# Kernel tuning notes

Hardware: AMD Instinct MI355X
Metric: run time of the kernel (lower is better)

Reference implementation:

```python
import jax, jax.numpy as jnp
import numpy as np

B, C, N, M, K = 8, 64, 8192, 2048, 16
FPS_RATIO, TAU = 0.7, 0.2


def setup_inputs() -> dict:
    key = jax.random.key(0)
    k1, k2 = jax.random.split(key)
    x = jax.random.normal(k1, (B, C, N), dtype=jnp.float32)
    pos = jax.random.normal(k2, (B, 3, N), dtype=jnp.float32)
    return {"x": x, "pos": pos, "m": M}


def _fps(pts, key, fps_m):
    # pts: [N, 3] -> farthest point sampling indices [fps_m]
    n = pts.shape[0]
    start = jax.random.randint(key, (), 0, n)
    d0 = jnp.full((n,), 1e10, dtype=jnp.float32)

    def step(carry, _):
        dist, last = carry
        d = jnp.sum((pts - pts[last]) ** 2, axis=1)  # [N]
        dist = jnp.minimum(dist, d)
        far = jnp.argmax(dist)
        return (dist, far), far

    (_, _), cents = jax.lax.scan(step, (d0, start), None, length=fps_m - 1)
    return jnp.concatenate([start[None], cents])


def _hybrid_idx(pos, m, fps_ratio, key):
    # pos: [B, 3, N] -> idx [B, m]  (FPS for fps_m points, random for the rest)
    b, _, n = pos.shape
    fps_m = max(1, int(m * fps_ratio))
    rand_m = m - fps_m
    pts = jnp.transpose(pos, (0, 2, 1))  # [B, N, 3]
    keys = jax.random.split(key, b)
    cents = jax.vmap(lambda p, k: _fps(p, k, fps_m))(pts, keys)  # [B, fps_m]
    if rand_m > 0:
        rkeys = jax.random.split(jax.random.fold_in(key, 1), b)
        rand = jax.vmap(lambda k: jax.random.permutation(k, n)[:rand_m])(rkeys)
        idx = jnp.concatenate([cents, rand], axis=1)
    else:
        idx = cents
    return idx[:, :m]


def _gather_neighbor(feat, idx):
    # feat: [B, C, N], idx: [B, m, k] -> [B, C, m, k]
    return jax.vmap(lambda f, i: f[:, i])(feat, idx)


def reference(x, pos, m):
    b = x.shape[0]
    idx = _hybrid_idx(pos, m, FPS_RATIO, jax.random.key(42))  # [B, m]
    pos_sub = jax.vmap(lambda p, i: p[:, i])(pos, idx)  # [B, 3, m]

    # KNN via squared distances (same ordering as euclidean cdist), no grad path
    ps = jax.lax.stop_gradient(jnp.transpose(pos_sub, (0, 2, 1)))  # [B, m, 3]
    pa = jax.lax.stop_gradient(jnp.transpose(pos, (0, 2, 1)))      # [B, N, 3]
    d2 = (jnp.sum(ps * ps, axis=-1)[:, :, None]
          + jnp.sum(pa * pa, axis=-1)[:, None, :]
          - 2.0 * jnp.einsum('bmd,bnd->bmn', ps, pa))  # [B, m, N]
    _, knn_idx = jax.lax.top_k(-d2, K)  # [B, m, K] smallest distances

    neigh_x = _gather_neighbor(x, knn_idx)      # [B, C, m, K]
    neigh_pos = _gather_neighbor(pos, knn_idx)  # [B, 3, m, K]

    d = jnp.linalg.norm(neigh_pos - pos_sub[..., None], axis=1)  # [B, m, K]
    d = jnp.maximum(d, 1e-6)
    w = jax.nn.softmax(-d / max(1e-6, TAU), axis=-1)  # [B, m, K]
    x_sub = jnp.sum(neigh_x * w[:, None, :, :], axis=-1)  # [B, C, m]
    return x_sub, pos_sub
```

## Files before the change

kernel.cpp:

```cpp
#include <hip/hip_runtime.h>

constexpr int NB   = 8;
constexpr int NC   = 64;
constexpr int NN   = 8192;
constexpr int NM   = 2048;
constexpr int NK   = 16;
constexpr int NFPS = 1433;
constexpr int NRAND = NM - NFPS;

constexpr size_t OFF_CTR   = 0;
constexpr size_t OFF_IDX   = 256;
constexpr size_t OFF_V1    = 66048;
constexpr size_t OFF_XT    = 1377280;

typedef float v2f __attribute__((ext_vector_type(2)));

struct TF { unsigned a, b; };

__device__ __forceinline__ TF tf2(unsigned k0, unsigned k1, unsigned c0, unsigned c1) {
  unsigned ks2 = k0 ^ k1 ^ 0x1BD11BDAu;
  unsigned x0 = c0 + k0;
  unsigned x1 = c1 + k1;
#define TF_R(r) { x0 += x1; x1 = (x1 << r) | (x1 >> (32 - r)); x1 ^= x0; }
  TF_R(13) TF_R(15) TF_R(26) TF_R(6)
  x0 += k1;  x1 += ks2 + 1u;
  TF_R(17) TF_R(29) TF_R(16) TF_R(24)
  x0 += ks2; x1 += k0 + 2u;
  TF_R(13) TF_R(15) TF_R(26) TF_R(6)
  x0 += k0;  x1 += k1 + 3u;
  TF_R(17) TF_R(29) TF_R(16) TF_R(24)
  x0 += k1;  x1 += ks2 + 4u;
  TF_R(13) TF_R(15) TF_R(26) TF_R(6)
  x0 += ks2; x1 += k0 + 5u;
#undef TF_R
  TF r; r.a = x0; r.b = x1; return r;
}

__device__ __forceinline__ float wave_max_dpp(float v) {
  int vi;
  vi = __builtin_amdgcn_update_dpp(__float_as_int(v), __float_as_int(v), 0x111, 0xf, 0xf, false);
  v = fmaxf(v, __int_as_float(vi));
  vi = __builtin_amdgcn_update_dpp(__float_as_int(v), __float_as_int(v), 0x112, 0xf, 0xf, false);
  v = fmaxf(v, __int_as_float(vi));
  vi = __builtin_amdgcn_update_dpp(__float_as_int(v), __float_as_int(v), 0x114, 0xf, 0xf, false);
  v = fmaxf(v, __int_as_float(vi));
  vi = __builtin_amdgcn_update_dpp(__float_as_int(v), __float_as_int(v), 0x118, 0xf, 0xf, false);
  v = fmaxf(v, __int_as_float(vi));
  vi = __builtin_amdgcn_update_dpp(__float_as_int(v), __float_as_int(v), 0x142, 0xa, 0xf, false);
  v = fmaxf(v, __int_as_float(vi));
  vi = __builtin_amdgcn_update_dpp(__float_as_int(v), __float_as_int(v), 0x143, 0xc, 0xf, false);
  v = fmaxf(v, __int_as_float(vi));
  return __int_as_float(__builtin_amdgcn_readlane(__float_as_int(v), 63));
}

__device__ __forceinline__ void poll_ge(unsigned* p, unsigned target) {
  while (__hip_atomic_load(p, __ATOMIC_RELAXED, __HIP_MEMORY_SCOPE_AGENT) < target)
    __builtin_amdgcn_s_sleep(32);
}
__device__ __forceinline__ int load_i(int* p) {
  return __hip_atomic_load(p, __ATOMIC_RELAXED, __HIP_MEMORY_SCOPE_AGENT);
}
__device__ __forceinline__ unsigned load_u(unsigned* p) {
  return __hip_atomic_load(p, __ATOMIC_RELAXED, __HIP_MEMORY_SCOPE_AGENT);
}

constexpr int FPS_BLKS = NB;
constexpr int NW = 256 - FPS_BLKS;
constexpr int TR_TILES = (NN / 32) * (NC / 32) * NB;
constexpr int KNN_GRPS = NB * NM / 4;

__global__ __launch_bounds__(256, 1) void mega_kernel(const float* __restrict__ pos,
                                                      const float* __restrict__ x,
                                                      int* __restrict__ idx,
                                                      unsigned* __restrict__ v1buf,
                                                      float* __restrict__ xT,
                                                      float* __restrict__ xOut,
                                                      float* __restrict__ posOut,
                                                      unsigned* __restrict__ ctrl) {
  __shared__ __align__(16) char smem[98432];
  const int bid = blockIdx.x;
  const int tid = threadIdx.x;
  unsigned* wbar    = ctrl;
  unsigned* fpsProg = ctrl + 16;
  unsigned* permFlg = ctrl + 32;
  unsigned* ticket  = ctrl + 48;

  if (bid < FPS_BLKS) {
    float* ldsX = (float*)smem;
    float* ldsY = (float*)(smem + 32768);
    float* ldsZ = (float*)(smem + 65536);
    float2 (*slot)[4] = (float2(*)[4])(smem + 98304);
    const int b = bid;
    const int wv = tid >> 6, lane = tid & 63;
    const float* pb = pos + (size_t)b * 3 * NN;
    v2f px[16], py[16], pz[16], dist[16];
    const int base = tid * 32;
    const float4* fx = (const float4*)(pb + base);
    const float4* fy = (const float4*)(pb + NN + base);
    const float4* fz = (const float4*)(pb + 2 * NN + base);
#pragma unroll
    for (int q = 0; q < 8; ++q) {
      float4 a = fx[q], c = fy[q], e = fz[q];
      px[2*q].x = a.x; px[2*q].y = a.y; px[2*q+1].x = a.z; px[2*q+1].y = a.w;
      py[2*q].x = c.x; py[2*q].y = c.y; py[2*q+1].x = c.z; py[2*q+1].y = c.w;
      pz[2*q].x = e.x; pz[2*q].y = e.y; pz[2*q+1].x = e.z; pz[2*q+1].y = e.w;
      ((float4*)(ldsX + base))[q] = a;
      ((float4*)(ldsY + base))[q] = c;
      ((float4*)(ldsZ + base))[q] = e;
    }
#pragma unroll
    for (int p = 0; p < 16; ++p) { dist[p].x = 1e10f; dist[p].y = 1e10f; }
    TF kb_ = tf2(0u, 42u, 0u, (unsigned)b);
    TF k2 = tf2(kb_.a, kb_.b, 0u, 1u);
    TF bt = tf2(k2.a, k2.b, 0u, 0u);
    int widx = (int)((bt.a ^ bt.b) & (unsigned)(NN - 1));
    if (tid == 0) {
      __hip_atomic_store(&idx[b * NM], widx, __ATOMIC_RELAXED, __HIP_MEMORY_SCOPE_AGENT);
      __hip_atomic_store(&fpsProg[b], 1u, __ATOMIC_RELEASE, __HIP_MEMORY_SCOPE_AGENT);
    }
    __syncthreads();
    float cx = ldsX[widx], cy = ldsY[widx], cz = ldsZ[widx];
    for (int it = 1; it < NFPS; ++it) {
      const int par = it & 1;
      float bestv = -1.0f; int bestS = 0;
      {
        v2f cx2; cx2.x = cx; cx2.y = cx;
        v2f cy2; cy2.x = cy; cy2.y = cy;
        v2f cz2; cz2.x = cz; cz2.y = cz;
#pragma unroll
        for (int p = 0; p < 16; ++p) {
#pragma clang fp contract(off)
          v2f dx = px[p] - cx2;
          v2f dy = py[p] - cy2;
          v2f dz = pz[p] - cz2;
          v2f d2 = (dx * dx + dy * dy) + dz * dz;
          float nd0 = fminf(dist[p].x, d2.x);
          float nd1 = fminf(dist[p].y, d2.y);
          dist[p].x = nd0; dist[p].y = nd1;
          bool c0 = nd0 > bestv;
          bestv = c0 ? nd0 : bestv;
          bestS = c0 ? 2*p : bestS;
          bool c1 = nd1 > bestv;
          bestv = c1 ? nd1 : bestv;
          bestS = c1 ? 2*p + 1 : bestS;
        }
      }
      const int gidx = base + bestS;
      const float wm = wave_max_dpp(bestv);
      unsigned long long msk = __ballot(bestv == wm);
      const int fl = (int)__builtin_ctzll(msk);
      const int widxw = __builtin_amdgcn_readlane(gidx, fl);
      if (lane == 0) slot[par][wv] = make_float2(wm, __int_as_float(widxw));
      __syncthreads();
      float2 s0 = slot[par][0], s1 = slot[par][1], s2 = slot[par][2], s3 = slot[par][3];
      if (s1.x > s0.x) s0 = s1;
      if (s3.x > s2.x) s2 = s3;
      if (s2.x > s0.x) s0 = s2;
      widx = __float_as_int(s0.y);
      cx = ldsX[widx]; cy = ldsY[widx]; cz = ldsZ[widx];
      if (tid == 0) {
        __hip_atomic_store(&idx[b * NM + it], widx, __ATOMIC_RELAXED, __HIP_MEMORY_SCOPE_AGENT);
        if ((it & 31) == 31)
          __hip_atomic_store(&fpsProg[b], (unsigned)(it + 1), __ATOMIC_RELEASE,
                             __HIP_MEMORY_SCOPE_AGENT);
      }
    }
    if (tid == 0)
      __hip_atomic_store(&fpsProg[b], (unsigned)NFPS, __ATOMIC_RELEASE,
                         __HIP_MEMORY_SCOPE_AGENT);
    return;
  }

  const int w = bid - FPS_BLKS;

  {
    float (*t)[33] = (float(*)[33])smem;
    const int tx = tid & 31, ty0 = tid >> 5;
    for (int tt = w; tt < TR_TILES; tt += NW) {
      const int n0 = (tt & 255) * 32;
      const int c0 = ((tt >> 8) & 1) * 32;
      const int bb = tt >> 9;
#pragma unroll
      for (int r = 0; r < 4; ++r) {
        const int ty = ty0 + r * 8;
        t[ty][tx] = x[((size_t)bb * NC + (c0 + ty)) * NN + n0 + tx];
      }
      __syncthreads();
#pragma unroll
      for (int r = 0; r < 4; ++r) {
        const int ty = ty0 + r * 8;
        xT[((size_t)bb * NN + (n0 + ty)) * NC + c0 + tx] = t[tx][ty];
      }
      __syncthreads();
    }
  }
  __threadfence();
  __syncthreads();
  if (tid == 0) {
    atomicAdd(wbar, 1u);
    while (__hip_atomic_load(wbar, __ATOMIC_RELAXED, __HIP_MEMORY_SCOPE_AGENT) < (unsigned)NW)
      __builtin_amdgcn_s_sleep(8);
  }
  __syncthreads();
  __threadfence();

  if (w < 16) {
    unsigned long long* s = (unsigned long long*)smem;
    const int b = w >> 1, r = w & 1;
    TF keyr = tf2(0u, 42u, 0u, 1u);
    TF rk = tf2(keyr.a, keyr.b, 0u, (unsigned)b);
    TF s1k = tf2(rk.a, rk.b, 0u, 1u);
    TF nk  = tf2(rk.a, rk.b, 0u, 0u);
    TF s2k = tf2(nk.a, nk.b, 0u, 1u);
    const unsigned ka = r ? s2k.a : s1k.a;
    const unsigned kb = r ? s2k.b : s1k.b;
    for (int i = tid; i < NN; i += 256) {
      TF t = tf2(ka, kb, 0u, (unsigned)i);
      s[i] = ((unsigned long long)(t.a ^ t.b) << 32) | (unsigned)i;
    }
    for (unsigned k = 2; k <= 8192u; k <<= 1) {
      for (unsigned j = k >> 1; j > 0; j >>= 1) {
        __syncthreads();
        for (unsigned t2 = (unsigned)tid; t2 < 4096u; t2 += 256u) {
          unsigned i = ((t2 & ~(j - 1u)) << 1) | (t2 & (j - 1u));
          unsigned p = i | j;
          bool up = ((i & k) == 0u);
          unsigned long long a = s[i], c = s[p];
          if ((a > c) == up) { s[i] = c; s[p] = a; }
        }
      }
    }
    __syncthreads();
    if (r == 0) {
      unsigned* v1 = v1buf + (size_t)b * NN;
      for (int i = tid; i < NN; i += 256)
        __hip_atomic_store(&v1[i], (unsigned)(s[i] & 0xffffffffu),
                           __ATOMIC_RELAXED, __HIP_MEMORY_SCOPE_AGENT);
    } else {
      for (int t2 = tid; t2 < NRAND; t2 += 256)
        __hip_atomic_store(&idx[b * NM + NFPS + t2], (int)(s[t2] & 0xffffffffu),
                           __ATOMIC_RELAXED, __HIP_MEMORY_SCOPE_AGENT);
    }
    __syncthreads();
    if (tid == 0)
      __hip_atomic_store(&permFlg[w], 1u, __ATOMIC_RELEASE, __HIP_MEMORY_SCOPE_AGENT);
  }
  __syncthreads();

  {
    unsigned long long (*lst)[NK][64] = (unsigned long long(*)[NK][64])smem;
    float (*tile)[4] = (float(*)[4])(smem + 32768);
    int* tkt = (int*)(smem + 33792);
    const int wv = tid >> 6, lane = tid & 63;
    for (;;) {
      __syncthreads();
      if (tid == 0) *tkt = (int)atomicAdd(ticket, 1u);
      __syncthreads();
      const int t = *tkt;
      if (t >= KNN_GRPS) break;
      int b, gm;
      if (t < 1016)      { gm = t >> 3;                  b = t & 7; }
      else if (t < 2240) { gm = 359 + ((t - 1016) >> 3); b = (t - 1016) & 7; }
      else               { gm = 127 + ((t - 2240) >> 3); b = (t - 2240) & 7; }
      const int mm = gm * 4 + wv;
      const float* pb = pos + (size_t)b * 3 * NN;
      int raw, id;
      if (mm < NFPS) {
        poll_ge(&fpsProg[b], (unsigned)(mm + 1));
        raw = load_i(&idx[b * NM + mm]);
        id = raw;
      } else {
        poll_ge(&permFlg[b * 2 + 1], 1u);
        raw = load_i(&idx[b * NM + mm]);
        poll_ge(&permFlg[b * 2 + 0], 1u);
        id = (int)load_u(&v1buf[(size_t)b * NN + raw]);
      }
      const float sx = pb[id], sy = pb[NN + id], sz = pb[2 * NN + id];
      const float sm = __fadd_rn(__fadd_rn(__fmul_rn(sx, sx), __fmul_rn(sy, sy)),
                                 __fmul_rn(sz, sz));
      float key[NK]; int kid[NK];
#pragma unroll
      for (int i = 0; i < NK; ++i) { key[i] = __int_as_float(0x7F800000); kid[i] = 0; }
      for (int tt2 = 0; tt2 < NN / 256; ++tt2) {
        const int n0 = tt2 * 256 + lane * 4;
        const float4 xv = *(const float4*)(pb + n0);
        const float4 yv = *(const float4*)(pb + NN + n0);
        const float4 zv = *(const float4*)(pb + 2 * NN + n0);
#pragma unroll
        for (int j = 0; j < 4; ++j) {
          const float xx = (j == 0) ? xv.x : (j == 1) ? xv.y : (j == 2) ? xv.z : xv.w;
          const float yy = (j == 0) ? yv.x : (j == 1) ? yv.y : (j == 2) ? yv.z : yv.w;
          const float zz = (j == 0) ? zv.x : (j == 1) ? zv.y : (j == 2) ? zv.z : zv.w;
          float sn = __fadd_rn(__fadd_rn(__fmul_rn(xx, xx), __fmul_rn(yy, yy)), __fmul_rn(zz, zz));
          float dt = __fadd_rn(__fadd_rn(__fmul_rn(sx, xx), __fmul_rn(sy, yy)), __fmul_rn(sz, zz));
          float d2 = __fsub_rn(__fadd_rn(sm, sn), __fmul_rn(2.0f, dt));
          const float ck = d2; const int ci = n0 + j;
#pragma unroll
          for (int i = NK - 1; i >= 1; --i) {
            float lo = key[i-1], hi = key[i];
            bool cLo = ck < lo, cHi = ck < hi;
            key[i] = __builtin_amdgcn_fmed3f(ck, lo, hi);
            kid[i] = cLo ? kid[i-1] : (cHi ? ci : kid[i]);
          }
          bool c0 = ck < key[0];
          kid[0] = c0 ? ci : kid[0];
          key[0] = fminf(key[0], ck);
        }
      }
#pragma unroll
      for (int i = 0; i < NK; ++i) {
        unsigned u = __float_as_uint(key[i]);
        u = (u & 0x80000000u) ? ~u : (u | 0x80000000u);
        lst[wv][i][lane] = ((unsigned long long)u << 32) | (unsigned)kid[i];
      }
      int ptr = 0;
      unsigned long long head = lst[wv][0][lane];
      unsigned myn = 0;
      for (int k = 0; k < NK; ++k) {
        unsigned long long mn = head;
#pragma unroll
        for (int off = 32; off > 0; off >>= 1) {
          unsigned long long o = __shfl_xor(mn, off, 64);
          if (o < mn) mn = o;
        }
        if (head == mn) { ++ptr; head = (ptr < NK) ? lst[wv][ptr][lane] : ~0ull; }
        if (lane == k) myn = (unsigned)(mn & 0xffffffffu);
      }
      const int kk = lane & 15;
      const int nk = (int)__shfl(myn, kk, 64);
      float dx = __fsub_rn(pb[nk], sx);
      float dy = __fsub_rn(pb[NN + nk], sy);
      float dz = __fsub_rn(pb[2 * NN + nk], sz);
      float dd = __fadd_rn(__fadd_rn(__fmul_rn(dx, dx), __fmul_rn(dy, dy)),
                           __fmul_rn(dz, dz));
      float d = __fsqrt_rn(dd);
      d = fmaxf(d, 1e-6f);
      float e = __fdiv_rn(0.0f - d, 0.2f);
      float mx = e;
#pragma unroll
      for (int off = 8; off > 0; off >>= 1) mx = fmaxf(mx, __shfl_xor(mx, off, 16));
      float ex = expf(__fsub_rn(e, mx));
      float sum = ex;
#pragma unroll
      for (int off = 8; off > 0; off >>= 1) sum = __fadd_rn(sum, __shfl_xor(sum, off, 16));
      float wgt = __fdiv_rn(ex, sum);
      float acc = 0.0f;
#pragma unroll
      for (int k = 0; k < NK; ++k) {
        float wk = __shfl(wgt, k, 64);
        int   nn = __shfl(nk, k, 64);
        acc = __fadd_rn(acc, __fmul_rn(wk, xT[((size_t)b * NN + nn) * NC + lane]));
      }
      tile[lane][wv] = acc;
      __syncthreads();
      {
        int c = tid >> 2, ml = tid & 3;
        xOut[((size_t)b * NC + c) * NM + gm * 4 + ml] = tile[c][ml];
      }
    }
  }

  for (int i = w * 256 + tid; i < NB * 3 * NM; i += NW * 256) {
    int mm = i & (NM - 1);
    int bd = i >> 11;
    int d = bd % 3, b = bd / 3;
    if (mm < NFPS) poll_ge(&fpsProg[b], (unsigned)(mm + 1));
    else { poll_ge(&permFlg[b * 2 + 1], 1u); poll_ge(&permFlg[b * 2 + 0], 1u); }
    int raw = load_i(&idx[b * NM + mm]);
    int id = (mm < NFPS) ? raw : (int)load_u(&v1buf[(size_t)b * NN + raw]);
    posOut[i] = pos[((size_t)b * 3 + d) * NN + id];
  }
}

extern "C" void kernel_launch(void* const* d_in, const int* in_sizes, int n_in,
                              void* d_out, int out_size, void* d_ws, size_t ws_size,
                              hipStream_t stream) {
  const float* x   = (const float*)d_in[0];
  const float* pos = (const float*)d_in[1];
  float* xOut   = (float*)d_out;
  float* posOut = xOut + (size_t)NB * NC * NM;

  char* w = (char*)d_ws;
  unsigned* ctrl = (unsigned*)(w + OFF_CTR);
  int*      idx  = (int*)(w + OFF_IDX);
  unsigned* v1   = (unsigned*)(w + OFF_V1);
  float*    xT   = (float*)(w + OFF_XT);

  hipMemsetAsync(w + OFF_CTR, 0, 256, stream);

  void* args[] = {(void*)&pos, (void*)&x, (void*)&idx, (void*)&v1,
                  (void*)&xT, (void*)&xOut, (void*)&posOut, (void*)&ctrl};
  hipError_t e = hipLaunchCooperativeKernel((const void*)mega_kernel, dim3(256), dim3(256),
                                            args, 0, stream);
  if (e != hipSuccess) {
    hipLaunchKernelGGL(mega_kernel, dim3(256), dim3(256), 0, stream,
                       pos, x, idx, v1, xT, xOut, posOut, ctrl);
  }
}
```

Baseline: 1.344 ms.

## Split FPS-dependent KNN queries across four waves and publish FPS progress less often

For the query range that depends on FPS results arriving late (points 508 through 1435), each ticket now covers a single query point. The block's four waves each scan a quarter of the N points, and their per-wave top-16 lists are merged through shared memory. The aim is to shorten the critical tail behind the serial FPS producer, because each late query now finishes about four times sooner once its centroid is published. FPS progress is also published every 128 iterations rather than every 32, which cuts atomic release stores. In exchange there are more tickets, an extra merge step and barrier per query, and consumers see coarser progress granularity.

Result: slower. 1.393 ms (+3.7%).

```diff
diff --git a/kernel.cpp b/kernel.cpp
--- a/kernel.cpp
+++ b/kernel.cpp
@@ -67,7 +67,9 @@
 constexpr int FPS_BLKS = NB;
 constexpr int NW = 256 - FPS_BLKS;
 constexpr int TR_TILES = (NN / 32) * (NC / 32) * NB;
-constexpr int KNN_GRPS = NB * NM / 4;
+constexpr int TKT_B0    = 1016;
+constexpr int TKT_C0    = 2240;
+constexpr int TKT_TOTAL = 2240 + 7424;
 
 __global__ __launch_bounds__(256, 1) void mega_kernel(const float* __restrict__ pos,
                                                       const float* __restrict__ x,
@@ -160,7 +162,7 @@
       cx = ldsX[widx]; cy = ldsY[widx]; cz = ldsZ[widx];
       if (tid == 0) {
         __hip_atomic_store(&idx[b * NM + it], widx, __ATOMIC_RELAXED, __HIP_MEMORY_SCOPE_AGENT);
-        if ((it & 31) == 31)
+        if ((it & 127) == 127)
           __hip_atomic_store(&fpsProg[b], (unsigned)(it + 1), __ATOMIC_RELEASE,
                              __HIP_MEMORY_SCOPE_AGENT);
       }
@@ -251,111 +253,222 @@
     unsigned long long (*lst)[NK][64] = (unsigned long long(*)[NK][64])smem;
     float (*tile)[4] = (float(*)[4])(smem + 32768);
     int* tkt = (int*)(smem + 33792);
+    unsigned long long* cm = (unsigned long long*)(smem + 33856);
     const int wv = tid >> 6, lane = tid & 63;
     for (;;) {
       __syncthreads();
       if (tid == 0) *tkt = (int)atomicAdd(ticket, 1u);
       __syncthreads();
       const int t = *tkt;
-      if (t >= KNN_GRPS) break;
-      int b, gm;
-      if (t < 1016)      { gm = t >> 3;                  b = t & 7; }
-      else if (t < 2240) { gm = 359 + ((t - 1016) >> 3); b = (t - 1016) & 7; }
-      else               { gm = 127 + ((t - 2240) >> 3); b = (t - 2240) & 7; }
-      const int mm = gm * 4 + wv;
-      const float* pb = pos + (size_t)b * 3 * NN;
-      int raw, id;
-      if (mm < NFPS) {
-        poll_ge(&fpsProg[b], (unsigned)(mm + 1));
-        raw = load_i(&idx[b * NM + mm]);
-        id = raw;
+      if (t >= TKT_TOTAL) break;
+      if (t < TKT_C0) {
+        int b, gm;
+        if (t < TKT_B0) { gm = t >> 3;                      b = t & 7; }
+        else            { gm = 359 + ((t - TKT_B0) >> 3);   b = (t - TKT_B0) & 7; }
+        const int mm = gm * 4 + wv;
+        const float* pb = pos + (size_t)b * 3 * NN;
+        int raw, id;
+        if (mm < NFPS) {
+          poll_ge(&fpsProg[b], (unsigned)(mm + 1));
+          raw = load_i(&idx[b * NM + mm]);
+          id = raw;
+        } else {
+          poll_ge(&permFlg[b * 2 + 1], 1u);
+          raw = load_i(&idx[b * NM + mm]);
+          poll_ge(&permFlg[b * 2 + 0], 1u);
+          id = (int)load_u(&v1buf[(size_t)b * NN + raw]);
+        }
+        const float sx = pb[id], sy = pb[NN + id], sz = pb[2 * NN + id];
+        const float sm = __fadd_rn(__fadd_rn(__fmul_rn(sx, sx), __fmul_rn(sy, sy)),
+                                   __fmul_rn(sz, sz));
+        float key[NK]; int kid[NK];
+#pragma unroll
+        for (int i = 0; i < NK; ++i) { key[i] = __int_as_float(0x7F800000); kid[i] = 0; }
+        for (int tt2 = 0; tt2 < NN / 256; ++tt2) {
+          const int n0 = tt2 * 256 + lane * 4;
+          const float4 xv = *(const float4*)(pb + n0);
+          const float4 yv = *(const float4*)(pb + NN + n0);
+          const float4 zv = *(const float4*)(pb + 2 * NN + n0);
+#pragma unroll
+          for (int j = 0; j < 4; ++j) {
+            const float xx = (j == 0) ? xv.x : (j == 1) ? xv.y : (j == 2) ? xv.z : xv.w;
+            const float yy = (j == 0) ? yv.x : (j == 1) ? yv.y : (j == 2) ? yv.z : yv.w;
+            const float zz = (j == 0) ? zv.x : (j == 1) ? zv.y : (j == 2) ? zv.z : zv.w;
+            float sn = __fadd_rn(__fadd_rn(__fmul_rn(xx, xx), __fmul_rn(yy, yy)), __fmul_rn(zz, zz));
+            float dt = __fadd_rn(__fadd_rn(__fmul_rn(sx, xx), __fmul_rn(sy, yy)), __fmul_rn(sz, zz));
+            float d2 = __fsub_rn(__fadd_rn(sm, sn), __fmul_rn(2.0f, dt));
+            const float ck = d2; const int ci = n0 + j;
+#pragma unroll
+            for (int i = NK - 1; i >= 1; --i) {
+              float lo = key[i-1], hi = key[i];
+              bool cLo = ck < lo, cHi = ck < hi;
+              key[i] = __builtin_amdgcn_fmed3f(ck, lo, hi);
+              kid[i] = cLo ? kid[i-1] : (cHi ? ci : kid[i]);
+            }
+            bool c0 = ck < key[0];
+            kid[0] = c0 ? ci : kid[0];
+            key[0] = fminf(key[0], ck);
+          }
+        }
+#pragma unroll
+        for (int i = 0; i < NK; ++i) {
+          unsigned u = __float_as_uint(key[i]);
+          u = (u & 0x80000000u) ? ~u : (u | 0x80000000u);
+          lst[wv][i][lane] = ((unsigned long long)u << 32) | (unsigned)kid[i];
+        }
+        int ptr = 0;
+        unsigned long long head = lst[wv][0][lane];
+        unsigned myn = 0;
+        for (int k = 0; k < NK; ++k) {
+          unsigned long long mn = head;
+#pragma unroll
+          for (int off = 32; off > 0; off >>= 1) {
+            unsigned long long o = __shfl_xor(mn, off, 64);
+            if (o < mn) mn = o;
+          }
+          if (head == mn) { ++ptr; head = (ptr < NK) ? lst[wv][ptr][lane] : ~0ull; }
+          if (lane == k) myn = (unsigned)(mn & 0xffffffffu);
+        }
+        const int kk = lane & 15;
+        const int nk = (int)__shfl(myn, kk, 64);
+        float dx = __fsub_rn(pb[nk], sx);
+        float dy = __fsub_rn(pb[NN + nk], sy);
+        float dz = __fsub_rn(pb[2 * NN + nk], sz);
+        float dd = __fadd_rn(__fadd_rn(__fmul_rn(dx, dx), __fmul_rn(dy, dy)),
+                             __fmul_rn(dz, dz));
+        float d = __fsqrt_rn(dd);
+        d = fmaxf(d, 1e-6f);
+        float e = __fdiv_rn(0.0f - d, 0.2f);
+        float mx = e;
+#pragma unroll
+        for (int off = 8; off > 0; off >>= 1) mx = fmaxf(mx, __shfl_xor(mx, off, 16));
+        float ex = expf(__fsub_rn(e, mx));
+        float sum = ex;
+#pragma unroll
+        for (int off = 8; off > 0; off >>= 1) sum = __fadd_rn(sum, __shfl_xor(sum, off, 16));
+        float wgt = __fdiv_rn(ex, sum);
+        float acc = 0.0f;
+#pragma unroll
+        for (int k = 0; k < NK; ++k) {
+          float wk = __shfl(wgt, k, 64);
+          int   nn = __shfl(nk, k, 64);
+          acc = __fadd_rn(acc, __fmul_rn(wk, xT[((size_t)b * NN + nn) * NC + lane]));
+        }
+        tile[lane][wv] = acc;
+        __syncthreads();
+        {
+          int c = tid >> 2, ml = tid & 3;
+          xOut[((size_t)b * NC + c) * NM + gm * 4 + ml] = tile[c][ml];
+        }
       } else {
-        poll_ge(&permFlg[b * 2 + 1], 1u);
-        raw = load_i(&idx[b * NM + mm]);
-        poll_ge(&permFlg[b * 2 + 0], 1u);
-        id = (int)load_u(&v1buf[(size_t)b * NN + raw]);
-      }
-      const float sx = pb[id], sy = pb[NN + id], sz = pb[2 * NN + id];
-      const float sm = __fadd_rn(__fadd_rn(__fmul_rn(sx, sx), __fmul_rn(sy, sy)),
-                                 __fmul_rn(sz, sz));
-      float key[NK]; int kid[NK];
-#pragma unroll
-      for (int i = 0; i < NK; ++i) { key[i] = __int_as_float(0x7F800000); kid[i] = 0; }
-      for (int tt2 = 0; tt2 < NN / 256; ++tt2) {
-        const int n0 = tt2 * 256 + lane * 4;
-        const float4 xv = *(const float4*)(pb + n0);
-        const float4 yv = *(const float4*)(pb + NN + n0);
-        const float4 zv = *(const float4*)(pb + 2 * NN + n0);
-#pragma unroll
-        for (int j = 0; j < 4; ++j) {
-          const float xx = (j == 0) ? xv.x : (j == 1) ? xv.y : (j == 2) ? xv.z : xv.w;
-          const float yy = (j == 0) ? yv.x : (j == 1) ? yv.y : (j == 2) ? yv.z : yv.w;
-          const float zz = (j == 0) ? zv.x : (j == 1) ? zv.y : (j == 2) ? zv.z : zv.w;
-          float sn = __fadd_rn(__fadd_rn(__fmul_rn(xx, xx), __fmul_rn(yy, yy)), __fmul_rn(zz, zz));
-          float dt = __fadd_rn(__fadd_rn(__fmul_rn(sx, xx), __fmul_rn(sy, yy)), __fmul_rn(sz, zz));
-          float d2 = __fsub_rn(__fadd_rn(sm, sn), __fmul_rn(2.0f, dt));
-          const float ck = d2; const int ci = n0 + j;
-#pragma unroll
-          for (int i = NK - 1; i >= 1; --i) {
-            float lo = key[i-1], hi = key[i];
-            bool cLo = ck < lo, cHi = ck < hi;
-            key[i] = __builtin_amdgcn_fmed3f(ck, lo, hi);
-            kid[i] = cLo ? kid[i-1] : (cHi ? ci : kid[i]);
+        const int tc = t - TKT_C0;
+        const int mm = 508 + (tc >> 3);
+        const int b  = tc & 7;
+        const float* pb = pos + (size_t)b * 3 * NN;
+        int raw, id;
+        if (mm < NFPS) {
+          poll_ge(&fpsProg[b], (unsigned)(mm + 1));
+          raw = load_i(&idx[b * NM + mm]);
+          id = raw;
+        } else {
+          poll_ge(&permFlg[b * 2 + 1], 1u);
+          raw = load_i(&idx[b * NM + mm]);
+          poll_ge(&permFlg[b * 2 + 0], 1u);
+          id = (int)load_u(&v1buf[(size_t)b * NN + raw]);
+        }
+        const float sx = pb[id], sy = pb[NN + id], sz = pb[2 * NN + id];
+        const float sm = __fadd_rn(__fadd_rn(__fmul_rn(sx, sx), __fmul_rn(sy, sy)),
+                                   __fmul_rn(sz, sz));
+        float key[NK]; int kid[NK];
+#pragma unroll
+        for (int i = 0; i < NK; ++i) { key[i] = __int_as_float(0x7F800000); kid[i] = 0; }
+        for (int tt2 = 0; tt2 < 8; ++tt2) {
+          const int n0 = wv * 2048 + tt2 * 256 + lane * 4;
+          const float4 xv = *(const float4*)(pb + n0);
+          const float4 yv = *(const float4*)(pb + NN + n0);
+          const float4 zv = *(const float4*)(pb + 2 * NN + n0);
+#pragma unroll
+          for (int j = 0; j < 4; ++j) {
+            const float xx = (j == 0) ? xv.x : (j == 1) ? xv.y : (j == 2) ? xv.z : xv.w;
+            const float yy = (j == 0) ? yv.x : (j == 1) ? yv.y : (j == 2) ? yv.z : yv.w;
+            const float zz = (j == 0) ? zv.x : (j == 1) ? zv.y : (j == 2) ? zv.z : zv.w;
+            float sn = __fadd_rn(__fadd_rn(__fmul_rn(xx, xx), __fmul_rn(yy, yy)), __fmul_rn(zz, zz));
+            float dt = __fadd_rn(__fadd_rn(__fmul_rn(sx, xx), __fmul_rn(sy, yy)), __fmul_rn(sz, zz));
+            float d2 = __fsub_rn(__fadd_rn(sm, sn), __fmul_rn(2.0f, dt));
+            const float ck = d2; const int ci = n0 + j;
+#pragma unroll
+            for (int i = NK - 1; i >= 1; --i) {
+              float lo = key[i-1], hi = key[i];
+              bool cLo = ck < lo, cHi = ck < hi;
+              key[i] = __builtin_amdgcn_fmed3f(ck, lo, hi);
+              kid[i] = cLo ? kid[i-1] : (cHi ? ci : kid[i]);
+            }
+            bool c0 = ck < key[0];
+            kid[0] = c0 ? ci : kid[0];
+            key[0] = fminf(key[0], ck);
           }
-          bool c0 = ck < key[0];
-          kid[0] = c0 ? ci : kid[0];
-          key[0] = fminf(key[0], ck);
-        }
-      }
-#pragma unroll
-      for (int i = 0; i < NK; ++i) {
-        unsigned u = __float_as_uint(key[i]);
-        u = (u & 0x80000000u) ? ~u : (u | 0x80000000u);
-        lst[wv][i][lane] = ((unsigned long long)u << 32) | (unsigned)kid[i];
-      }
-      int ptr = 0;
-      unsigned long long head = lst[wv][0][lane];
-      unsigned myn = 0;
-      for (int k = 0; k < NK; ++k) {
-        unsigned long long mn = head;
-#pragma unroll
-        for (int off = 32; off > 0; off >>= 1) {
-          unsigned long long o = __shfl_xor(mn, off, 64);
-          if (o < mn) mn = o;
-        }
-        if (head == mn) { ++ptr; head = (ptr < NK) ? lst[wv][ptr][lane] : ~0ull; }
-        if (lane == k) myn = (unsigned)(mn & 0xffffffffu);
-      }
-      const int kk = lane & 15;
-      const int nk = (int)__shfl(myn, kk, 64);
-      float dx = __fsub_rn(pb[nk], sx);
-      float dy = __fsub_rn(pb[NN + nk], sy);
-      float dz = __fsub_rn(pb[2 * NN + nk], sz);
-      float dd = __fadd_rn(__fadd_rn(__fmul_rn(dx, dx), __fmul_rn(dy, dy)),
-                           __fmul_rn(dz, dz));
-      float d = __fsqrt_rn(dd);
-      d = fmaxf(d, 1e-6f);
-      float e = __fdiv_rn(0.0f - d, 0.2f);
-      float mx = e;
-#pragma unroll
-      for (int off = 8; off > 0; off >>= 1) mx = fmaxf(mx, __shfl_xor(mx, off, 16));
-      float ex = expf(__fsub_rn(e, mx));
-      float sum = ex;
-#pragma unroll
-      for (int off = 8; off > 0; off >>= 1) sum = __fadd_rn(sum, __shfl_xor(sum, off, 16));
-      float wgt = __fdiv_rn(ex, sum);
-      float acc = 0.0f;
-#pragma unroll
-      for (int k = 0; k < NK; ++k) {
-        float wk = __shfl(wgt, k, 64);
-        int   nn = __shfl(nk, k, 64);
-        acc = __fadd_rn(acc, __fmul_rn(wk, xT[((size_t)b * NN + nn) * NC + lane]));
-      }
-      tile[lane][wv] = acc;
-      __syncthreads();
-      {
-        int c = tid >> 2, ml = tid & 3;
-        xOut[((size_t)b * NC + c) * NM + gm * 4 + ml] = tile[c][ml];
+        }
+#pragma unroll
+        for (int i = 0; i < NK; ++i) {
+          unsigned u = __float_as_uint(key[i]);
+          u = (u & 0x80000000u) ? ~u : (u | 0x80000000u);
+          lst[wv][i][lane] = ((unsigned long long)u << 32) | (unsigned)kid[i];
+        }
+        int ptr = 0;
+        unsigned long long head = lst[wv][0][lane];
+        unsigned long long myc = ~0ull;
+        for (int k = 0; k < NK; ++k) {
+          unsigned long long mn = head;
+#pragma unroll
+          for (int off = 32; off > 0; off >>= 1) {
+            unsigned long long o = __shfl_xor(mn, off, 64);
+            if (o < mn) mn = o;
+          }
+          if (head == mn) { ++ptr; head = (ptr < NK) ? lst[wv][ptr][lane] : ~0ull; }
+          if (lane == k) myc = mn;
+        }
+        if (lane < NK) cm[wv * NK + lane] = myc;
+        __syncthreads();
+        if (wv == 0) {
+          unsigned long long mine = cm[lane];
+          unsigned myn = 0;
+          for (int k = 0; k < NK; ++k) {
+            unsigned long long mn = mine;
+#pragma unroll
+            for (int off = 32; off > 0; off >>= 1) {
+              unsigned long long o = __shfl_xor(mn, off, 64);
+              if (o < mn) mn = o;
+            }
+            if (mine == mn) mine = ~0ull;
+            if (lane == k) myn = (unsigned)(mn & 0xffffffffu);
+          }
+          const int kk = lane & 15;
+          const int nk = (int)__shfl(myn, kk, 64);
+          float dx = __fsub_rn(pb[nk], sx);
+          float dy = __fsub_rn(pb[NN + nk], sy);
+          float dz = __fsub_rn(pb[2 * NN + nk], sz);
+          float dd = __fadd_rn(__fadd_rn(__fmul_rn(dx, dx), __fmul_rn(dy, dy)),
+                               __fmul_rn(dz, dz));
+          float d = __fsqrt_rn(dd);
+          d = fmaxf(d, 1e-6f);
+          float e = __fdiv_rn(0.0f - d, 0.2f);
+          float mx = e;
+#pragma unroll
+          for (int off = 8; off > 0; off >>= 1) mx = fmaxf(mx, __shfl_xor(mx, off, 16));
+          float ex = expf(__fsub_rn(e, mx));
+          float sum = ex;
+#pragma unroll
+          for (int off = 8; off > 0; off >>= 1) sum = __fadd_rn(sum, __shfl_xor(sum, off, 16));
+          float wgt = __fdiv_rn(ex, sum);
+          float acc = 0.0f;
+#pragma unroll
+          for (int k = 0; k < NK; ++k) {
+            float wk = __shfl(wgt, k, 64);
+            int   nn = __shfl(nk, k, 64);
+            acc = __fadd_rn(acc, __fmul_rn(wk, xT[((size_t)b * NN + nn) * NC + lane]));
+          }
+          xOut[((size_t)b * NC + lane) * NM + mm] = acc;
+        }
       }
     }
   }
```
